# Kernel optimization log

Measured on AMD Instinct MI355X. Metric: run time of the kernel, lower is better.

The kernel has to match this reference:

```python
import jax, jax.numpy as jnp
import numpy as np

BS, SEQ, D_MODEL = 4, 1024, 4096
N_Q_HEADS, N_KV_HEADS, D_K, D_V = 32, 8, 128, 128
ROPE_BASE = 10000.0


def _rotate_half(x):
    x1, x2 = jnp.split(x, 2, axis=-1)
    return jnp.concatenate([-x2, x1], axis=-1)


def _apply_rope(x, pos0):
    # x: [bs, heads, seq, d]; positions pos0 .. pos0+seq-1
    d = x.shape[-1]
    seq = x.shape[2]
    inv_freq = 1.0 / (ROPE_BASE ** (jnp.arange(0, d, 2, dtype=jnp.float32) / d))  # [d/2]
    pos = (pos0 + jnp.arange(seq)).astype(jnp.float32)  # [seq]
    ang = pos[:, None] * inv_freq[None, :]  # [seq, d/2]
    cos = jnp.concatenate([jnp.cos(ang), jnp.cos(ang)], axis=-1)  # [seq, d]
    sin = jnp.concatenate([jnp.sin(ang), jnp.sin(ang)], axis=-1)
    return x * cos[None, None] + _rotate_half(x) * sin[None, None]


def setup_inputs() -> dict:
    key = jax.random.key(0)
    ks = jax.random.split(key, 8)
    w_scale = 0.02  # keep logits in a sane range (original uses raw normal init)
    return {
        "query": jax.random.normal(ks[0], (BS, SEQ, D_MODEL), dtype=jnp.float32),
        "key": jax.random.normal(ks[1], (BS, SEQ, D_MODEL), dtype=jnp.float32),
        "value": jax.random.normal(ks[2], (BS, SEQ, D_MODEL), dtype=jnp.float32),
        "mask": jnp.zeros((BS, SEQ, SEQ), dtype=jnp.float32),
        "wq": jax.random.normal(ks[3], (D_MODEL, N_Q_HEADS * D_K), dtype=jnp.float32) * w_scale,
        "wk": jax.random.normal(ks[4], (D_MODEL, N_KV_HEADS * D_K), dtype=jnp.float32) * w_scale,
        "wv": jax.random.normal(ks[5], (D_MODEL, N_KV_HEADS * D_V), dtype=jnp.float32) * w_scale,
        "wo": jax.random.normal(ks[6], (N_Q_HEADS * D_V, D_MODEL), dtype=jnp.float32) * w_scale,
        "curr_seq_pos": 0,
    }


def reference(query, key, value, mask, wq, wk, wv, wo, curr_seq_pos):
    bs, sq, _ = query.shape
    n_groups = N_Q_HEADS // N_KV_HEADS
    # projections -> [bs, heads, seq, d]
    q = (query @ wq).reshape(bs, sq, N_Q_HEADS, D_K).transpose((0, 2, 1, 3))
    sk = key.shape[1]
    k = (key @ wk).reshape(bs, sk, N_KV_HEADS, 1, D_K)
    k = jnp.repeat(k, n_groups, axis=3).reshape(bs, sk, N_Q_HEADS, D_K).transpose((0, 2, 1, 3))
    v = (value @ wv).reshape(bs, sk, N_KV_HEADS, 1, D_V)
    v = jnp.repeat(v, n_groups, axis=3).reshape(bs, sk, N_Q_HEADS, D_V).transpose((0, 2, 1, 3))
    scale = jnp.sqrt(jnp.float32(D_K))
    q = _apply_rope(q, curr_seq_pos)
    k = _apply_rope(k, curr_seq_pos)
    # [bs, h, sq, sk]
    raw = jnp.einsum("bhqd,bhkd->bhqk", q, k) / scale
    masked = raw + mask[:bs, None, curr_seq_pos:curr_seq_pos + sq, :sk]
    attn = jax.nn.softmax(masked, axis=-1)
    out = jnp.einsum("bhqk,bhkd->bhqd", attn, v)
    out = out.transpose((0, 2, 1, 3)).reshape(bs, sq, N_Q_HEADS * D_V)
    return out @ wo
```

## Files before the change

kernel.cpp:

```cpp
#include <hip/hip_runtime.h>


using ushort = unsigned short;
typedef __attribute__((ext_vector_type(8))) short short8;
typedef __attribute__((ext_vector_type(4))) short short4v;
typedef __attribute__((ext_vector_type(4))) float f32x4;

__device__ __forceinline__ ushort f2bf(float x) {
  unsigned int u = __float_as_uint(x);
  u += 0x7FFFu + ((u >> 16) & 1u);
  return (ushort)(u >> 16);
}
__device__ __forceinline__ float bf2f(ushort h) {
  return __uint_as_float(((unsigned int)h) << 16);
}

__device__ __forceinline__ void async_copy16(const void* g, void* l) {
  __builtin_amdgcn_global_load_lds((const __attribute__((address_space(1))) void*)g,
                                   (__attribute__((address_space(3))) void*)l, 16, 0, 0);
}

__global__ __launch_bounds__(256)
void cvt_f32_bf16(const float* __restrict__ in, ushort* __restrict__ out, int n4) {
  const int i = blockIdx.x * 256 + threadIdx.x;
  if (i < n4) {
    const float4 f = ((const float4*)in)[i];
    short4v v;
    v[0] = (short)f2bf(f.x); v[1] = (short)f2bf(f.y);
    v[2] = (short)f2bf(f.z); v[3] = (short)f2bf(f.w);
    ((short4v*)out)[i] = v;
  }
}

__global__ __launch_bounds__(256)
void transpose_cvt(const float* __restrict__ B, ushort* __restrict__ Bt, int N) {
  __shared__ ushort t[64][72];
  const int n0 = blockIdx.x * 64, k0 = blockIdx.y * 64;
  const int tid = threadIdx.x;
  const int r = tid >> 3, c8 = (tid & 7) * 8;
#pragma unroll
  for (int p = 0; p < 2; p++) {
    const float* src = B + (size_t)(k0 + r + p * 32) * N + n0 + c8;
    const float4 f0 = *(const float4*)src;
    const float4 f1 = *(const float4*)(src + 4);
    ushort* d = &t[r + p * 32][c8];
    d[0] = f2bf(f0.x); d[1] = f2bf(f0.y); d[2] = f2bf(f0.z); d[3] = f2bf(f0.w);
    d[4] = f2bf(f1.x); d[5] = f2bf(f1.y); d[6] = f2bf(f1.z); d[7] = f2bf(f1.w);
  }
  __syncthreads();
#pragma unroll
  for (int p = 0; p < 2; p++) {
    const int n = r + p * 32;
    short8 o;
#pragma unroll
    for (int j = 0; j < 8; j++) o[j] = (short)t[c8 + j][n];
    *(short8*)(Bt + (size_t)(n0 + n) * 4096 + k0 + c8) = o;
  }
}

template <int MODE, bool AF32>
__global__ __launch_bounds__(256, 2)
void gemm_bt(const float* __restrict__ Af, const float* __restrict__ A2f,
             const ushort* __restrict__ Abf, const ushort* __restrict__ Bt,
             ushort* __restrict__ C, ushort* __restrict__ C2,
             float* __restrict__ Cf, int N, float scale) {
  constexpr int K = 4096;
  __shared__ alignas(16) ushort As[128 * 32];
  __shared__ alignas(16) ushort Bs[128 * 32];
  const int tid = threadIdx.x;
  const int wave = tid >> 6, lane = tid & 63;
  const int quad = lane >> 4, l16 = lane & 15;
  const int m0 = blockIdx.y * 128, n0 = blockIdx.x * 128;
  const int wm = (wave & 1) * 64, wn = (wave >> 1) * 64;

  const size_t aoff = (size_t)(m0 + wave * 16 + (lane >> 2)) * K + (lane & 3) * 8;
  const float* gAf = nullptr;
  const ushort* gAb = nullptr;
  if constexpr (AF32) {
    const float* Ause = Af;
    if constexpr (MODE == 4) {
      if (n0 >= 1024) Ause = A2f;
    }
    gAf = Ause + aoff;
  } else {
    gAb = Abf + aoff;
  }
  const ushort* gB = Bt + (size_t)(n0 + wave * 16 + (lane >> 2)) * K + (lane & 3) * 8;
  ushort* lA = As + wave * 512;
  ushort* lB = Bs + wave * 512;
  constexpr size_t rstep = (size_t)64 * K;

  f32x4 acc[4][4] = {};

  for (int kt = 0; kt < K; kt += 32) {
    if constexpr (AF32) {
      const float4 a0 = *(const float4*)(gAf + kt);
      const float4 a1 = *(const float4*)(gAf + kt + 4);
      const float4 b0 = *(const float4*)(gAf + rstep + kt);
      const float4 b1 = *(const float4*)(gAf + rstep + kt + 4);
      short8 v0, v1;
      v0[0] = (short)f2bf(a0.x); v0[1] = (short)f2bf(a0.y);
      v0[2] = (short)f2bf(a0.z); v0[3] = (short)f2bf(a0.w);
      v0[4] = (short)f2bf(a1.x); v0[5] = (short)f2bf(a1.y);
      v0[6] = (short)f2bf(a1.z); v0[7] = (short)f2bf(a1.w);
      v1[0] = (short)f2bf(b0.x); v1[1] = (short)f2bf(b0.y);
      v1[2] = (short)f2bf(b0.z); v1[3] = (short)f2bf(b0.w);
      v1[4] = (short)f2bf(b1.x); v1[5] = (short)f2bf(b1.y);
      v1[6] = (short)f2bf(b1.z); v1[7] = (short)f2bf(b1.w);
      *(short8*)(lA + lane * 8) = v0;
      *(short8*)(lA + 2048 + lane * 8) = v1;
    } else {
      async_copy16(gAb + kt, lA);
      async_copy16(gAb + rstep + kt, lA + 2048);
    }
    async_copy16(gB + kt, lB);
    async_copy16(gB + rstep + kt, lB + 2048);
    __syncthreads();
    short8 af[4], bfrag[4];
#pragma unroll
    for (int i = 0; i < 4; i++) {
      af[i] = *(const short8*)(As + (wm + i * 16 + l16) * 32 + quad * 8);
      bfrag[i] = *(const short8*)(Bs + (wn + i * 16 + l16) * 32 + quad * 8);
    }
#pragma unroll
    for (int i = 0; i < 4; i++)
#pragma unroll
      for (int j = 0; j < 4; j++)
        acc[i][j] = __builtin_amdgcn_mfma_f32_16x16x32_bf16(af[i], bfrag[j],
                                                            acc[i][j], 0, 0, 0);
    __syncthreads();
  }

#pragma unroll
  for (int i = 0; i < 4; i++) {
#pragma unroll
    for (int j = 0; j < 4; j++) {
      const int mb = m0 + wm + i * 16 + quad * 4;
      const int n = n0 + wn + j * 16 + l16;
#pragma unroll
      for (int r = 0; r < 4; r++) {
        const int m = mb + r;
        const float xv = acc[i][j][r] * scale;
        if constexpr (MODE == 0) {
          Cf[(size_t)m * N + n] = xv;
        } else if constexpr (MODE == 1) {
          const int b = m >> 10, s = m & 1023, hh = n >> 7, d = n & 127;
          C[(((size_t)b * 32 + hh) * 1024 + s) * 128 + d] = f2bf(xv);
        } else {
          const int b = m >> 10, s = m & 1023;
          if (n < 1024) {
            const int hh = n >> 7, d = n & 127;
            C[(((size_t)b * 8 + hh) * 1024 + s) * 128 + d] = f2bf(xv);
          } else {
            const int n2 = n - 1024;
            const int hh = n2 >> 7, d = n2 & 127;
            C2[(((size_t)b * 8 + hh) * 128 + d) * 1024 + s] = f2bf(xv);
          }
        }
      }
    }
  }
}

__global__ void rope_kernel(ushort* __restrict__ Q, ushort* __restrict__ Kh,
                            const int* __restrict__ posp, int nQrows) {
  const int row = blockIdx.x;
  const int d = threadIdx.x;
  ushort* p = (row < nQrows) ? (Q + (size_t)row * 128)
                             : (Kh + (size_t)(row - nQrows) * 128);
  const int s = row & 1023;
  const float pos = (float)(s + posp[0]);
  const float inv = exp2f((float)d * (-13.287712379549449f / 64.0f));
  const float ang = pos * inv;
  const float cs = cosf(ang), sn = sinf(ang);
  const float x1 = bf2f(p[d]);
  const float x2 = bf2f(p[d + 64]);
  p[d] = f2bf(x1 * cs - x2 * sn);
  p[d + 64] = f2bf(x2 * cs + x1 * sn);
}

__global__ __launch_bounds__(256, 2)
void attn_kernel(const ushort* __restrict__ Qh, const ushort* __restrict__ Kh,
                 const ushort* __restrict__ Vt, const ushort* __restrict__ Mk,
                 ushort* __restrict__ Oh) {
  __shared__ alignas(16) ushort Qs[64 * 128];
  __shared__ alignas(16) ushort Ks[64 * 128];
  __shared__ alignas(16) ushort Vs[128 * 64];
  __shared__ alignas(16) ushort Ms[64 * 64];
  ushort* Ps = Ks;
  const int b = blockIdx.z, h = blockIdx.y;
  const int q0 = blockIdx.x * 64;
  const int hkv = h >> 2;
  const int tid = threadIdx.x;
  const int wave = tid >> 6, lane = tid & 63;
  const int quad = lane >> 4, l16 = lane & 15;

  const ushort* Qg = Qh + (((size_t)b * 32 + h) * 1024 + q0) * 128;
  const ushort* Kg = Kh + ((size_t)b * 8 + hkv) * (size_t)(1024 * 128);
  const ushort* Vg = Vt + ((size_t)b * 8 + hkv) * (size_t)(128 * 1024);
  const ushort* Mg = Mk + ((size_t)b * 1024 + q0) * 1024;

#pragma unroll
  for (int c = 0; c < 4; c++) {
    const int i = wave * 4 + c;
    const int row = i * 4 + (lane >> 4);
    const int kc = (lane & 15) ^ (c * 4 + (lane >> 4));
    async_copy16(Qg + (size_t)row * 128 + kc * 8, Qs + i * 512);
  }

  float m_i[4], l_i[4];
#pragma unroll
  for (int r = 0; r < 4; r++) { m_i[r] = -1e30f; l_i[r] = 0.0f; }
  f32x4 acc_o[8] = {};

  const int vr = lane >> 3;
  const int vkc = (lane & 7) ^ (vr & 7);

  for (int kt = 0; kt < 1024; kt += 64) {
#pragma unroll
    for (int c = 0; c < 4; c++) {
      const int i = wave * 4 + c;
      const int row = i * 4 + (lane >> 4);
      const int kc = (lane & 15) ^ (c * 4 + (lane >> 4));
      async_copy16(Kg + (size_t)(kt + row) * 128 + kc * 8, Ks + i * 512);
    }
#pragma unroll
    for (int c = 0; c < 4; c++) {
      const int i = wave * 4 + c;
      async_copy16(Vg + (size_t)(i * 8 + vr) * 1024 + kt + vkc * 8, Vs + i * 512);
    }
#pragma unroll
    for (int c = 0; c < 2; c++)
      async_copy16(Mg + (size_t)(wave * 8 + c * 32 + vr) * 1024 + kt + (lane & 7) * 8,
                   Ms + wave * 512 + c * 2048);
    __syncthreads();

    f32x4 s[4] = {};
    const int qrow = (wave * 16 + l16) * 128;
#pragma unroll
    for (int ks = 0; ks < 4; ks++) {
      const int ko = ((ks * 4 + quad) ^ l16) * 8;
      const short8 aq = *(const short8*)(Qs + qrow + ko);
#pragma unroll
      for (int nt = 0; nt < 4; nt++) {
        const short8 bk = *(const short8*)(Ks + (nt * 16 + l16) * 128 + ko);
        s[nt] = __builtin_amdgcn_mfma_f32_16x16x32_bf16(aq, bk, s[nt], 0, 0, 0);
      }
    }
    __syncthreads();

#pragma unroll
    for (int nt = 0; nt < 4; nt++)
#pragma unroll
      for (int r = 0; r < 4; r++)
        s[nt][r] += bf2f(Ms[(wave * 16 + quad * 4 + r) * 64 + nt * 16 + l16]);

    float al[4];
#pragma unroll
    for (int r = 0; r < 4; r++) {
      float mx = fmaxf(fmaxf(s[0][r], s[1][r]), fmaxf(s[2][r], s[3][r]));
#pragma unroll
      for (int off = 1; off < 16; off <<= 1) mx = fmaxf(mx, __shfl_xor(mx, off));
      const float mnew = fmaxf(m_i[r], mx);
      al[r] = __expf(m_i[r] - mnew);
      float sum = 0.0f;
#pragma unroll
      for (int nt = 0; nt < 4; nt++) {
        const float pv = __expf(s[nt][r] - mnew);
        s[nt][r] = pv;
        sum += pv;
      }
#pragma unroll
      for (int off = 1; off < 16; off <<= 1) sum += __shfl_xor(sum, off);
      l_i[r] = l_i[r] * al[r] + sum;
      m_i[r] = mnew;
    }
#pragma unroll
    for (int dt = 0; dt < 8; dt++)
#pragma unroll
      for (int r = 0; r < 4; r++) acc_o[dt][r] *= al[r];

#pragma unroll
    for (int nt = 0; nt < 4; nt++)
#pragma unroll
      for (int r = 0; r < 4; r++)
        Ps[wave * 1152 + (quad * 4 + r) * 72 + nt * 16 + l16] = f2bf(s[nt][r]);
    __asm__ volatile("s_waitcnt lgkmcnt(0)" ::: "memory");

#pragma unroll
    for (int kk = 0; kk < 2; kk++) {
      const short8 ap = *(const short8*)(Ps + wave * 1152 + l16 * 72 + kk * 32 + quad * 8);
#pragma unroll
      for (int dt = 0; dt < 8; dt++) {
        const int vo = ((kk * 4 + quad) ^ (l16 & 7)) * 8;
        const short8 bv = *(const short8*)(Vs + (dt * 16 + l16) * 64 + vo);
        acc_o[dt] = __builtin_amdgcn_mfma_f32_16x16x32_bf16(ap, bv, acc_o[dt], 0, 0, 0);
      }
    }
    __syncthreads();
  }

  ushort* Og = Oh + ((size_t)b * 1024 + q0 + wave * 16) * 4096 + h * 128;
#pragma unroll
  for (int r = 0; r < 4; r++) {
    const float inv = 1.0f / l_i[r];
#pragma unroll
    for (int dt = 0; dt < 8; dt++)
      Og[(size_t)(quad * 4 + r) * 4096 + dt * 16 + l16] = f2bf(acc_o[dt][r] * inv);
  }
}

extern "C" void kernel_launch(void* const* d_in, const int* in_sizes, int n_in,
                              void* d_out, int out_size, void* d_ws, size_t ws_size,
                              hipStream_t stream) {
  (void)in_sizes; (void)n_in; (void)out_size; (void)ws_size;
  const float* query = (const float*)d_in[0];
  const float* key = (const float*)d_in[1];
  const float* value = (const float*)d_in[2];
  const float* mask = (const float*)d_in[3];
  const float* wq = (const float*)d_in[4];
  const float* wk = (const float*)d_in[5];
  const float* wv = (const float*)d_in[6];
  const float* wo = (const float*)d_in[7];
  const int* pos = (const int*)d_in[8];
  float* out = (float*)d_out;

  char* ws = (char*)d_ws;
  const size_t MB = 1024 * 1024;
  ushort* wqT = (ushort*)(ws + 0 * MB);
  ushort* Ohb = (ushort*)(ws + 0 * MB);
  ushort* Qhb = (ushort*)(ws + 32 * MB);
  ushort* woT = (ushort*)(ws + 32 * MB);
  ushort* wkvT = (ushort*)(ws + 64 * MB);
  ushort* Khb = (ushort*)(ws + 80 * MB);
  ushort* Vtb = (ushort*)(ws + 88 * MB);
  ushort* mbf = (ushort*)(ws + 96 * MB);

  dim3 blk(256);
  cvt_f32_bf16<<<dim3(4096), blk, 0, stream>>>(mask, mbf, 1048576);

  transpose_cvt<<<dim3(64, 64), blk, 0, stream>>>(wq, wqT, 4096);
  gemm_bt<1, true><<<dim3(32, 32), blk, 0, stream>>>(
      query, nullptr, nullptr, wqT, Qhb, nullptr, nullptr, 4096, 0.08838834764831845f);

  transpose_cvt<<<dim3(16, 64), blk, 0, stream>>>(wk, wkvT, 1024);
  transpose_cvt<<<dim3(16, 64), blk, 0, stream>>>(wv, wkvT + (size_t)1024 * 4096, 1024);
  gemm_bt<4, true><<<dim3(16, 32), blk, 0, stream>>>(
      key, value, nullptr, wkvT, Khb, Vtb, nullptr, 2048, 1.0f);

  rope_kernel<<<dim3(131072 + 32768), dim3(64), 0, stream>>>(Qhb, Khb, pos, 131072);

  attn_kernel<<<dim3(16, 32, 4), blk, 0, stream>>>(Qhb, Khb, Vtb, mbf, Ohb);

  transpose_cvt<<<dim3(64, 64), blk, 0, stream>>>(wo, woT, 4096);
  gemm_bt<0, false><<<dim3(32, 32), blk, 0, stream>>>(
      nullptr, nullptr, Ohb, woT, nullptr, nullptr, out, 4096, 1.0f);
}
```

Measured before the change: 1.045 ms.

## Fuse RoPE into Q/K projection GEMM epilogue and pre-convert query to bf16

```diff
diff --git a/kernel.cpp b/kernel.cpp
--- a/kernel.cpp
+++ b/kernel.cpp
@@ -63,7 +63,8 @@
 void gemm_bt(const float* __restrict__ Af, const float* __restrict__ A2f,
              const ushort* __restrict__ Abf, const ushort* __restrict__ Bt,
              ushort* __restrict__ C, ushort* __restrict__ C2,
-             float* __restrict__ Cf, int N, float scale) {
+             float* __restrict__ Cf, const int* __restrict__ posp,
+             int N, float scale) {
   constexpr int K = 4096;
   __shared__ alignas(16) ushort As[128 * 32];
   __shared__ alignas(16) ushort Bs[128 * 32];
@@ -71,7 +72,7 @@
   const int wave = tid >> 6, lane = tid & 63;
   const int quad = lane >> 4, l16 = lane & 15;
   const int m0 = blockIdx.y * 128, n0 = blockIdx.x * 128;
-  const int wm = (wave & 1) * 64, wn = (wave >> 1) * 64;
+  const int wm = (wave & 1) * 64, wn2 = (wave >> 1) * 32;
 
   const size_t aoff = (size_t)(m0 + wave * 16 + (lane >> 2)) * K + (lane & 3) * 8;
   const float* gAf = nullptr;
@@ -120,7 +121,8 @@
 #pragma unroll
     for (int i = 0; i < 4; i++) {
       af[i] = *(const short8*)(As + (wm + i * 16 + l16) * 32 + quad * 8);
-      bfrag[i] = *(const short8*)(Bs + (wn + i * 16 + l16) * 32 + quad * 8);
+      bfrag[i] = *(const short8*)(
+          Bs + (wn2 + (i & 1) * 16 + (i >> 1) * 64 + l16) * 32 + quad * 8);
     }
 #pragma unroll
     for (int i = 0; i < 4; i++)
@@ -131,52 +133,64 @@
     __syncthreads();
   }
 
-#pragma unroll
-  for (int i = 0; i < 4; i++) {
-#pragma unroll
-    for (int j = 0; j < 4; j++) {
-      const int mb = m0 + wm + i * 16 + quad * 4;
-      const int n = n0 + wn + j * 16 + l16;
-#pragma unroll
-      for (int r = 0; r < 4; r++) {
-        const int m = mb + r;
-        const float xv = acc[i][j][r] * scale;
-        if constexpr (MODE == 0) {
-          Cf[(size_t)m * N + n] = xv;
-        } else if constexpr (MODE == 1) {
-          const int b = m >> 10, s = m & 1023, hh = n >> 7, d = n & 127;
-          C[(((size_t)b * 32 + hh) * 1024 + s) * 128 + d] = f2bf(xv);
-        } else {
-          const int b = m >> 10, s = m & 1023;
-          if (n < 1024) {
-            const int hh = n >> 7, d = n & 127;
-            C[(((size_t)b * 8 + hh) * 1024 + s) * 128 + d] = f2bf(xv);
-          } else {
-            const int n2 = n - 1024;
-            const int hh = n2 >> 7, d = n2 & 127;
-            C2[(((size_t)b * 8 + hh) * 128 + d) * 1024 + s] = f2bf(xv);
+  if constexpr (MODE == 0) {
+#pragma unroll
+    for (int i = 0; i < 4; i++)
+#pragma unroll
+      for (int j = 0; j < 4; j++) {
+        const int n = n0 + wn2 + (j & 1) * 16 + (j >> 1) * 64 + l16;
+        const int mb = m0 + wm + i * 16 + quad * 4;
+#pragma unroll
+        for (int r = 0; r < 4; r++)
+          Cf[(size_t)(mb + r) * N + n] = acc[i][j][r] * scale;
+      }
+  } else {
+    const bool kv_v = (MODE == 4) && (n0 >= 1024);
+    if (!kv_v) {
+      const int pos0 = posp[0];
+      const int h = (MODE == 1) ? (n0 >> 7) : (n0 >> 7);
+      const int NH = (MODE == 1) ? 32 : 8;
+      constexpr float lgbase = -0.20762050593045983f;
+      float invf[2];
+      invf[0] = exp2f((float)(wn2 + l16) * lgbase);
+      invf[1] = exp2f((float)(wn2 + 16 + l16) * lgbase);
+#pragma unroll
+      for (int i = 0; i < 4; i++) {
+#pragma unroll
+        for (int r = 0; r < 4; r++) {
+          const int m = m0 + wm + i * 16 + quad * 4 + r;
+          const int s = m & 1023, bb = m >> 10;
+          const float p = (float)(s + pos0);
+          ushort* row = C + (((size_t)bb * NH + h) * 1024 + s) * 128;
+#pragma unroll
+          for (int jj = 0; jj < 2; jj++) {
+            float sn, cs;
+            sincosf(p * invf[jj], &sn, &cs);
+            const float x1 = acc[i][jj][r] * scale;
+            const float x2 = acc[i][jj + 2][r] * scale;
+            const int dlo = wn2 + jj * 16 + l16;
+            row[dlo] = f2bf(x1 * cs - x2 * sn);
+            row[dlo + 64] = f2bf(x2 * cs + x1 * sn);
           }
         }
       }
-    }
-  }
-}
-
-__global__ void rope_kernel(ushort* __restrict__ Q, ushort* __restrict__ Kh,
-                            const int* __restrict__ posp, int nQrows) {
-  const int row = blockIdx.x;
-  const int d = threadIdx.x;
-  ushort* p = (row < nQrows) ? (Q + (size_t)row * 128)
-                             : (Kh + (size_t)(row - nQrows) * 128);
-  const int s = row & 1023;
-  const float pos = (float)(s + posp[0]);
-  const float inv = exp2f((float)d * (-13.287712379549449f / 64.0f));
-  const float ang = pos * inv;
-  const float cs = cosf(ang), sn = sinf(ang);
-  const float x1 = bf2f(p[d]);
-  const float x2 = bf2f(p[d + 64]);
-  p[d] = f2bf(x1 * cs - x2 * sn);
-  p[d + 64] = f2bf(x2 * cs + x1 * sn);
+    } else {
+      const int hh = (n0 - 1024) >> 7;
+#pragma unroll
+      for (int i = 0; i < 4; i++)
+#pragma unroll
+        for (int j = 0; j < 4; j++) {
+          const int d = wn2 + (j & 1) * 16 + (j >> 1) * 64 + l16;
+          const int mb = m0 + wm + i * 16 + quad * 4;
+#pragma unroll
+          for (int r = 0; r < 4; r++) {
+            const int m = mb + r;
+            const int bb = m >> 10, s = m & 1023;
+            C2[(((size_t)bb * 8 + hh) * 128 + d) * 1024 + s] = f2bf(acc[i][j][r]);
+          }
+        }
+    }
+  }
 }
 
 __global__ __launch_bounds__(256, 2)
@@ -327,32 +341,33 @@
 
   char* ws = (char*)d_ws;
   const size_t MB = 1024 * 1024;
-  ushort* wqT = (ushort*)(ws + 0 * MB);
-  ushort* Ohb = (ushort*)(ws + 0 * MB);
-  ushort* Qhb = (ushort*)(ws + 32 * MB);
-  ushort* woT = (ushort*)(ws + 32 * MB);
-  ushort* wkvT = (ushort*)(ws + 64 * MB);
-  ushort* Khb = (ushort*)(ws + 80 * MB);
-  ushort* Vtb = (ushort*)(ws + 88 * MB);
+  ushort* qb = (ushort*)(ws + 0 * MB);
+  ushort* Khb = (ushort*)(ws + 0 * MB);
+  ushort* Vtb = (ushort*)(ws + 8 * MB);
+  ushort* wqT = (ushort*)(ws + 32 * MB);
+  ushort* wkvT = (ushort*)(ws + 32 * MB);
+  ushort* Ohb = (ushort*)(ws + 32 * MB);
+  ushort* Qhb = (ushort*)(ws + 64 * MB);
+  ushort* woT = (ushort*)(ws + 64 * MB);
   ushort* mbf = (ushort*)(ws + 96 * MB);
 
   dim3 blk(256);
   cvt_f32_bf16<<<dim3(4096), blk, 0, stream>>>(mask, mbf, 1048576);
+  cvt_f32_bf16<<<dim3(16384), blk, 0, stream>>>(query, qb, 4194304);
 
   transpose_cvt<<<dim3(64, 64), blk, 0, stream>>>(wq, wqT, 4096);
-  gemm_bt<1, true><<<dim3(32, 32), blk, 0, stream>>>(
-      query, nullptr, nullptr, wqT, Qhb, nullptr, nullptr, 4096, 0.08838834764831845f);
+  gemm_bt<1, false><<<dim3(32, 32), blk, 0, stream>>>(
+      nullptr, nullptr, qb, wqT, Qhb, nullptr, nullptr, pos, 4096,
+      0.08838834764831845f);
 
   transpose_cvt<<<dim3(16, 64), blk, 0, stream>>>(wk, wkvT, 1024);
   transpose_cvt<<<dim3(16, 64), blk, 0, stream>>>(wv, wkvT + (size_t)1024 * 4096, 1024);
   gemm_bt<4, true><<<dim3(16, 32), blk, 0, stream>>>(
-      key, value, nullptr, wkvT, Khb, Vtb, nullptr, 2048, 1.0f);
-
-  rope_kernel<<<dim3(131072 + 32768), dim3(64), 0, stream>>>(Qhb, Khb, pos, 131072);
+      key, value, nullptr, wkvT, Khb, Vtb, nullptr, pos, 2048, 1.0f);
 
   attn_kernel<<<dim3(16, 32, 4), blk, 0, stream>>>(Qhb, Khb, Vtb, mbf, Ohb);
 
   transpose_cvt<<<dim3(64, 64), blk, 0, stream>>>(wo, woT, 4096);
   gemm_bt<0, false><<<dim3(32, 32), blk, 0, stream>>>(
-      nullptr, nullptr, Ohb, woT, nullptr, nullptr, out, 4096, 1.0f);
-}
+      nullptr, nullptr, Ohb, woT, nullptr, nullptr, out, pos, 4096, 1.0f);
+}
```

Result: faster. 971.1 us (-7.0%).
